# Kernel optimization log

Hardware: AMD Instinct MI355X
Metric: run time of the kernel (lower is better)

The kernel has to match this reference:

```python
import jax, jax.numpy as jnp
import numpy as np

ALPHA = 0.05   # propalpha
GDEP = 2       # gcn_depth
DIL = 2        # new_dilation
KSET = (2, 3, 6, 7)

def _dconv(x, w, b, d):
    # Conv2d(c_in, c_out, (1, k), dilation=(1, d), padding='same'), NCHW layout
    k = w.shape[-1]
    tot = d * (k - 1)
    lo = tot // 2
    y = jax.lax.conv_general_dilated(x, w, (1, 1), ((0, 0), (lo, tot - lo)),
                                     rhs_dilation=(1, d),
                                     dimension_numbers=('NCHW', 'OIHW', 'NCHW'))
    return y + b[None, :, None, None]

def _inception(x, ws, bs):
    # 'same' padding keeps seq_len for every branch, so the tail-slice is a no-op
    return jnp.concatenate([_dconv(x, w, b, DIL) for w, b in zip(ws, bs)], axis=1)

def _gcn(Hf, Aoff, W, b, n):
    # PyG GCNConv with unit edge weights (no edge_weight passed) and remaining self-loops:
    # out = D^-1/2 (A_off + I_R)^T D^-1/2 (Hf @ W^T) + b, where only rows < n carry edges.
    XW = Hf @ W.T
    deg = jnp.ones((Hf.shape[0],), Hf.dtype).at[:n].add(jnp.sum(Aoff, axis=0))
    dis = jax.lax.rsqrt(deg)
    out = XW / deg[:, None]                                           # self-loop term
    out = out.at[:n].add(dis[:n, None] * (Aoff.T @ (dis[:n, None] * XW[:n])))
    return out + b[None, :]

def _mixprop(X, A, gws, gbs, mw, mb):
    B, C, n, L = X.shape
    # dense_to_sparse ignores weights here (none passed to GCNConv) -> binary adjacency;
    # add_remaining_self_loops replaces any diagonal entries, so zero the diagonal.
    Aoff = (A != 0).astype(X.dtype) * (1.0 - jnp.eye(n, dtype=X.dtype))
    H = X
    hops = [X]
    for i in range(GDEP):
        Hf = H.reshape(B * L, C * n)   # torch row-major reshape, replicated exactly
        H1 = _gcn(Hf, Aoff, gws[i], gbs[i], n)
        H = ALPHA * X + H1.reshape(B, C, n, L)
        hops.append(H)
    Hc = jnp.concatenate(hops, axis=1)  # (B, (GDEP+1)*C, n, L)
    return jnp.einsum('bixl,oi->boxl', Hc, mw) + mb[None, :, None, None]

def _layernorm(x, w, b, idx, eps=1e-5):
    # F.layer_norm over all of x.shape[1:] with node-indexed affine params
    mu = jnp.mean(x, axis=(1, 2, 3), keepdims=True)
    var = jnp.var(x, axis=(1, 2, 3), keepdims=True)
    xh = (x - mu) * jax.lax.rsqrt(var + eps)
    return xh * w[:, idx, :][None] + b[:, idx, :][None]

def _forward(x, x_skip, A, idx, fws, fbs, gws, gbs, skip_w, skip_b,
             mp1_gw, mp1_gb, mp1_mw, mp1_mb, mp2_gw, mp2_gb, mp2_mw, mp2_mb,
             ln_w, ln_b):
    x_res = x
    xf = jnp.tanh(_inception(x, fws, fbs))
    xg = jax.nn.sigmoid(_inception(x, gws, gbs))
    x = xf * xg  # gated dilated temporal conv (dropout is an eval-mode no-op)
    x_skip = jnp.einsum('bixl,oi->boxl', x, skip_w) + skip_b[None, :, None, None] + x_skip
    x = (_mixprop(x, A, mp1_gw, mp1_gb, mp1_mw, mp1_mb)
         + _mixprop(x.swapaxes(0, 0), A.T, mp2_gw, mp2_gb, mp2_mw, mp2_mb))
    x = x + x_res[..., -x.shape[3]:]
    x = _layernorm(x, ln_w, ln_b, idx)
    return x, x_skip

def setup_inputs():
    key = jax.random.key(0)
    ks = jax.random.split(key, 32)
    B, C, N, L, SKIP = 16, 32, 128, 128, 64
    F = C * N
    co = C // len(KSET)
    d = {}
    d['x'] = jax.random.normal(ks[0], (B, C, N, L), jnp.float32)
    d['x_skip'] = jax.random.normal(ks[1], (B, SKIP, N, L), jnp.float32)
    d['A'] = jax.random.uniform(ks[2], (N, N), jnp.float32)
    d['idx'] = jnp.arange(N, dtype=jnp.int32)
    i = 3
    for pre in ('f', 'g'):
        for k in KSET:
            d[pre + 'w' + str(k)] = jax.random.normal(ks[i], (co, C, 1, k), jnp.float32) * float(1.0 / np.sqrt(C * k))
            d[pre + 'b' + str(k)] = jax.random.uniform(ks[i + 1], (co,), jnp.float32)
            i += 2
    d['skip_w'] = jax.random.normal(ks[i], (SKIP, C), jnp.float32) * float(1.0 / np.sqrt(C)); i += 1
    d['skip_b'] = jax.random.uniform(ks[i], (SKIP,), jnp.float32); i += 1
    for mp in ('mp1', 'mp2'):
        d[mp + '_gw'] = jax.random.normal(ks[i], (GDEP, F, F), jnp.float32) * float(1.0 / np.sqrt(F)); i += 1
        d[mp + '_gb'] = jnp.zeros((GDEP, F), jnp.float32)
        d[mp + '_mw'] = jax.random.normal(ks[i], (C, (GDEP + 1) * C), jnp.float32) * float(1.0 / np.sqrt((GDEP + 1) * C)); i += 1
        d[mp + '_mb'] = jax.random.uniform(ks[i], (C,), jnp.float32); i += 1
    d['ln_w'] = jnp.ones((C, N, L), jnp.float32)
    d['ln_b'] = jnp.zeros((C, N, L), jnp.float32)
    return d

def reference(x, x_skip, A, idx, fw2, fb2, fw3, fb3, fw6, fb6, fw7, fb7,
              gw2, gb2, gw3, gb3, gw6, gb6, gw7, gb7, skip_w, skip_b,
              mp1_gw, mp1_gb, mp1_mw, mp1_mb, mp2_gw, mp2_gb, mp2_mw, mp2_mb,
              ln_w, ln_b):
    return _forward(x, x_skip, A, idx,
                    [fw2, fw3, fw6, fw7], [fb2, fb3, fb6, fb7],
                    [gw2, gw3, gw6, gw7], [gb2, gb3, gb6, gb7],
                    skip_w, skip_b, mp1_gw, mp1_gb, mp1_mw, mp1_mb,
                    mp2_gw, mp2_gb, mp2_mw, mp2_mb, ln_w, ln_b)
```

## Files before the change

### kernel.cpp

```cpp
#include <hip/hip_runtime.h>
#include <stdint.h>

typedef unsigned short u16;
typedef unsigned int   u32;
typedef __attribute__((ext_vector_type(4))) float f32x4;
typedef __attribute__((ext_vector_type(8))) short bf16x8;

__device__ __forceinline__ u16 f2bf(float f) {
    u32 i = __float_as_uint(f);
    u32 r = (i + 0x7fffu + ((i >> 16) & 1u)) >> 16;
    return (u16)r;
}
__device__ __forceinline__ float bf2f(u16 u) {
    return __uint_as_float(((u32)u) << 16);
}
__device__ __forceinline__ u32 cvt2bf(float a, float b) {
    u32 r;
    asm("v_cvt_pk_bf16_f32 %0, %1, %2" : "=v"(r) : "v"(a), "v"(b));
    return r;
}

#define GLOAD16(g, l) __builtin_amdgcn_global_load_lds( \
    (const __attribute__((address_space(1))) void*)(g), \
    (__attribute__((address_space(3))) void*)(l), 16, 0, 0)

__global__ void k_prep(const float* __restrict__ A, float* dis1, float* inv1,
                       float* dis2, float* inv2)
{
    int r = threadIdx.x;
    if (r >= 128) return;
    int cc = 0, cr = 0;
    for (int j = 0; j < 128; ++j) {
        if (j == r) continue;
        if (A[(j << 7) + r] != 0.f) cc++;
        if (A[(r << 7) + j] != 0.f) cr++;
    }
    float d1 = 1.f + (float)cc, d2 = 1.f + (float)cr;
    dis1[r] = rsqrtf(d1); inv1[r] = 1.f / d1;
    dis2[r] = rsqrtf(d2); inv2[r] = 1.f / d2;
}

__global__ __launch_bounds__(256)
void k_wcvt2(const float* __restrict__ W0, const float* __restrict__ W1,
             u16* __restrict__ Wb0, u16* __restrict__ Wb1)
{
    int half = blockIdx.x >> 13;
    const float* W = half ? W1 : W0;
    u16* Wb = half ? Wb1 : Wb0;
    size_t e = ((size_t)(blockIdx.x & 8191) * 256 + threadIdx.x) * 8;
    f32x4 a = *(const f32x4*)(W + e);
    f32x4 b = *(const f32x4*)(W + e + 4);
    uint4 r;
    r.x = cvt2bf(a[0], a[1]); r.y = cvt2bf(a[2], a[3]);
    r.z = cvt2bf(b[0], b[1]); r.w = cvt2bf(b[2], b[3]);
    *(uint4*)(Wb + e) = r;
}

__global__ __launch_bounds__(512, 1)
void k_gemm2g(const u16* __restrict__ A0, const u16* __restrict__ A1,
              const u16* __restrict__ B0, const u16* __restrict__ B1,
              const u16* __restrict__ Gres,
              const float* __restrict__ gb0, const float* __restrict__ gb1,
              u16* __restrict__ Ha, u16* __restrict__ Hb,
              float* __restrict__ XW0a, float* __restrict__ XW0b)
{
    __shared__ alignas(16) u16 LDS[65536];
    const int NT = 128;
    const int tid  = threadIdx.x;
    const int lane = tid & 63;
    const int wid  = tid >> 6;
    const int wr = wid >> 2, wc = wid & 3;

    const int bid = blockIdx.x;
    const int swz = (bid & 7) * 32 + (bid >> 3);
    const int z   = swz >> 7;
    const int rem = swz & 127;
    const int bm = (rem >> 4) * 256;
    const int bn = (rem & 15) * 256;

    const u16* Ap = (z ? A1 : A0) + (size_t)bm * 4096;
    const u16* Bp = (z ? B1 : B0) + (size_t)bn * 4096;

    int aoff[8];
    #pragma unroll
    for (int i = 0; i < 8; ++i) {
        int ra = wr * 128 + i * 16 + (lane & 15);
        int sp = (lane >> 4) ^ ((ra >> 1) & 3);
        aoff[i] = ra * 32 + sp * 8;
    }
    int boff[4];
    #pragma unroll
    for (int j = 0; j < 4; ++j) {
        int rb = wc * 64 + j * 16 + (lane & 15);
        int sp = (lane >> 4) ^ ((rb >> 1) & 3);
        boff[j] = rb * 32 + sp * 8;
    }

    f32x4 acc[8][4] = {};

    auto stage = [&](int t) {
        const int k0  = t << 5;
        const int buf = (t & 3) << 14;
        #pragma unroll
        for (int h = 0; h < 2; ++h) {
            const int ch = tid + h * 512;
            const int r  = ch >> 2;
            const int sl = (ch & 3) ^ ((r >> 1) & 3);
            GLOAD16(Ap + (size_t)r * 4096 + k0 + sl * 8, LDS + buf + ch * 8);
            GLOAD16(Bp + (size_t)r * 4096 + k0 + sl * 8, LDS + buf + 8192 + ch * 8);
        }
    };
    auto compute = [&](int t) {
        const u16* base = LDS + ((t & 3) << 14);
        bf16x8 af[8], bv[4];
        #pragma unroll
        for (int i = 0; i < 8; ++i) af[i] = *(const bf16x8*)(base + aoff[i]);
        #pragma unroll
        for (int j = 0; j < 4; ++j) bv[j] = *(const bf16x8*)(base + 8192 + boff[j]);
        #pragma unroll
        for (int i = 0; i < 8; ++i)
            #pragma unroll
            for (int j = 0; j < 4; ++j)
                acc[i][j] = __builtin_amdgcn_mfma_f32_16x16x32_bf16(af[i], bv[j], acc[i][j], 0, 0, 0);
    };

    stage(0); stage(1); stage(2);
    asm volatile("s_waitcnt vmcnt(8)" ::: "memory");
    __syncthreads();

    int t = 0;
    for (; t < NT - 3; ++t) {
        stage(t + 3);
        compute(t);
        asm volatile("s_waitcnt vmcnt(8)" ::: "memory");
        __syncthreads();
    }
    compute(t);
    asm volatile("s_waitcnt vmcnt(4)" ::: "memory");
    __syncthreads(); ++t;
    compute(t);
    asm volatile("s_waitcnt vmcnt(0)" ::: "memory");
    __syncthreads(); ++t;
    compute(t);

    const int orow = (lane >> 4) * 4, ocol = lane & 15;
    const float* gbv = z ? gb1 : gb0;
    u16* H = z ? Hb : Ha;

    #pragma unroll
    for (int j = 0; j < 4; ++j) {
        const int o = bn + wc * 64 + j * 16 + ocol;
        const float gbo = gbv[o];
        #pragma unroll
        for (int i = 0; i < 8; ++i) {
            const int rbase = bm + wr * 128 + i * 16 + orow;
            #pragma unroll
            for (int v = 0; v < 4; ++v) {
                const size_t e = (size_t)(rbase + v) * 4096 + o;
                float g = bf2f(Gres[e]);
                H[e] = f2bf(__fmaf_rn(0.05f, g, acc[i][j][v] + gbo));
            }
        }
    }
    if (bm == 0 && wr == 0) {
        float* XW0 = z ? XW0b : XW0a;
        #pragma unroll
        for (int i = 0; i < 8; ++i) {
            #pragma unroll
            for (int j = 0; j < 4; ++j) {
                float* cp = XW0 + (size_t)(i * 16 + orow) * 4096 + (bn + wc * 64 + j * 16 + ocol);
                #pragma unroll
                for (int v = 0; v < 4; ++v)
                    cp[(size_t)v * 4096] = acc[i][j][v];
            }
        }
    }
}

__global__ __launch_bounds__(256)
void k_gcnfix(const float* __restrict__ XW0a, const float* __restrict__ XW0b,
              const u16* __restrict__ G, const float* __restrict__ Af,
              const float* __restrict__ dis1, const float* __restrict__ inv1,
              const float* __restrict__ dis2, const float* __restrict__ inv2,
              const float* __restrict__ gb0, const float* __restrict__ gb1,
              u16* __restrict__ Ha, u16* __restrict__ Hb)
{
    const int prob = blockIdx.x >> 9;
    const int rem  = blockIdx.x & 511;
    const int t4 = rem * 256 + threadIdx.x;
    const int r = t4 >> 10, og = (t4 & 1023) << 2;
    const float* XW0 = prob ? XW0b : XW0a;
    const float* dis = prob ? dis2 : dis1;
    const float* inv = prob ? inv2 : inv1;
    const float* gb  = prob ? gb1  : gb0;
    u16* H = prob ? Hb : Ha;

    const size_t e = ((size_t)r << 12) + og;
    f32x4 xw = *(const f32x4*)(XW0 + e);
    f32x4 s = {0.f, 0.f, 0.f, 0.f};
    for (int j = 0; j < 128; ++j) {
        float av = prob ? Af[(r << 7) + j] : Af[(j << 7) + r];
        float wv = ((av != 0.f) && (j != r)) ? dis[j] : 0.f;
        f32x4 xv = *(const f32x4*)(XW0 + ((size_t)j << 12) + og);
        #pragma unroll
        for (int q = 0; q < 4; ++q) s[q] = __fmaf_rn(wv, xv[q], s[q]);
    }
    const float iv = inv[r], dr = dis[r];
    f32x4 gb4 = *(const f32x4*)(gb + og);
    uint2 gv = *(const uint2*)(G + e);
    float g0 = __uint_as_float(gv.x << 16), g1 = __uint_as_float(gv.x & 0xffff0000u);
    float g2 = __uint_as_float(gv.y << 16), g3 = __uint_as_float(gv.y & 0xffff0000u);
    float y0 = __fmaf_rn(0.05f, g0, __fmaf_rn(dr, s[0], xw[0] * iv) + gb4[0]);
    float y1 = __fmaf_rn(0.05f, g1, __fmaf_rn(dr, s[1], xw[1] * iv) + gb4[1]);
    float y2 = __fmaf_rn(0.05f, g2, __fmaf_rn(dr, s[2], xw[2] * iv) + gb4[2]);
    float y3 = __fmaf_rn(0.05f, g3, __fmaf_rn(dr, s[3], xw[3] * iv) + gb4[3]);
    uint2 rr;
    rr.x = cvt2bf(y0, y1);
    rr.y = cvt2bf(y2, y3);
    *(uint2*)(H + e) = rr;
}

__device__ __forceinline__ constexpr int wbase_of(int k) {
    return k == 2 ? 0 : k == 3 ? 520 : k == 6 ? 1296 : 2840;
}
__device__ __forceinline__ constexpr int ob_of(int k) {
    return k == 2 ? 0 : k == 3 ? 8 : k == 6 ? 16 : 24;
}

template<int K_>
__device__ __forceinline__ void conv_phase(const float* __restrict__ xsb,
                                           const float* __restrict__ wfp,
                                           const float* __restrict__ wgp,
                                           float fb, float gb,
                                           u16* __restrict__ Gp)
{
    float accf[8], accg[8];
    #pragma unroll
    for (int i = 0; i < 8; ++i) { accf[i] = fb; accg[i] = gb; }
    for (int c = 0; c < 32; ++c) {
        float xw[24];
        const float* xr = xsb + c * 144;
        #pragma unroll
        for (int q = 0; q < 6; ++q) {
            f32x4 v = *(const f32x4*)(xr + q * 4);
            xw[q * 4 + 0] = v[0]; xw[q * 4 + 1] = v[1];
            xw[q * 4 + 2] = v[2]; xw[q * 4 + 3] = v[3];
        }
        float wfj[K_], wgj[K_];
        const float* wfc = wfp + c * K_;
        const float* wgc = wgp + c * K_;
        #pragma unroll
        for (int j = 0; j < K_; ++j) { wfj[j] = wfc[j]; wgj[j] = wgc[j]; }
        #pragma unroll
        for (int li = 0; li < 8; ++li) {
            #pragma unroll
            for (int j = 0; j < K_; ++j) {
                float xv = xw[li + 8 - (K_ - 1) + 2 * j];
                accf[li] = __fmaf_rn(xv, wfj[j], accf[li]);
                accg[li] = __fmaf_rn(xv, wgj[j], accg[li]);
            }
        }
    }
    u16 o8[8];
    #pragma unroll
    for (int i = 0; i < 8; ++i) {
        float e2 = __expf(2.f * accf[i]);
        float th = 1.f - __fdividef(2.f, e2 + 1.f);
        float sg = __fdividef(1.f, 1.f + __expf(-accg[i]));
        o8[i] = f2bf(th * sg);
    }
    uint4 u;
    u.x = o8[0] | ((u32)o8[1] << 16); u.y = o8[2] | ((u32)o8[3] << 16);
    u.z = o8[4] | ((u32)o8[5] << 16); u.w = o8[6] | ((u32)o8[7] << 16);
    *(uint4*)Gp = u;
}

template<int KA, int KB>
__device__ __forceinline__ void wave_pair(const float* __restrict__ xs,
                                          const float* __restrict__ wfl,
                                          const float* __restrict__ wgl,
                                          const float* __restrict__ fbl,
                                          const float* __restrict__ gbl,
                                          int oo, int lL, int b, int n,
                                          u16* __restrict__ G)
{
    {
        constexpr int BS = wbase_of(KA), ST = 32 * KA + 1, OB = ob_of(KA);
        const int o = OB + oo, l0 = lL * 8;
        conv_phase<KA>(xs + l0, wfl + BS + oo * ST, wgl + BS + oo * ST,
                       fbl[o], gbl[o],
                       G + (((size_t)(b * 32 + o) * 128 + n) * 128 + l0));
    }
    {
        constexpr int BS = wbase_of(KB), ST = 32 * KB + 1, OB = ob_of(KB);
        const int o = OB + oo, l0 = 64 + lL * 8;
        conv_phase<KB>(xs + l0, wfl + BS + oo * ST, wgl + BS + oo * ST,
                       fbl[o], gbl[o],
                       G + (((size_t)(b * 32 + o) * 128 + n) * 128 + l0));
    }
}

__global__ __launch_bounds__(256)
void k_incep(const float* __restrict__ x,
             const float* __restrict__ fw2p, const float* __restrict__ fw3p,
             const float* __restrict__ fw6p, const float* __restrict__ fw7p,
             const float* __restrict__ fb2p, const float* __restrict__ fb3p,
             const float* __restrict__ fb6p, const float* __restrict__ fb7p,
             const float* __restrict__ gw2p, const float* __restrict__ gw3p,
             const float* __restrict__ gw6p, const float* __restrict__ gw7p,
             const float* __restrict__ gb2p, const float* __restrict__ gb3p,
             const float* __restrict__ gb6p, const float* __restrict__ gb7p,
             u16* __restrict__ G)
{
    __shared__ alignas(16) float xs[32 * 144];
    __shared__ float wfl[4640], wgl[4640];
    __shared__ float fbl[32], gbl[32];
    const int tid = threadIdx.x;
    const int b = blockIdx.x >> 7, n = blockIdx.x & 127;

    for (int i = tid; i < 32 * 144; i += 256) xs[i] = 0.f;
    for (int g = tid; g < 4608; g += 256) {
        int rel, k, woff;
        const float *pf, *pg;
        if (g < 512)       { rel = g;        k = 2; woff = 0;    pf = fw2p; pg = gw2p; }
        else if (g < 1280) { rel = g - 512;  k = 3; woff = 520;  pf = fw3p; pg = gw3p; }
        else if (g < 2816) { rel = g - 1280; k = 6; woff = 1296; pf = fw6p; pg = gw6p; }
        else               { rel = g - 2816; k = 7; woff = 2840; pf = fw7p; pg = gw7p; }
        int ck = 32 * k;
        int oo = rel / ck, rem = rel % ck;
        int dst = woff + oo * (ck + 1) + rem;
        wfl[dst] = pf[rel];
        wgl[dst] = pg[rel];
    }
    if (tid < 32) {
        int br = tid >> 3, oo = tid & 7;
        const float* pf = br == 0 ? fb2p : br == 1 ? fb3p : br == 2 ? fb6p : fb7p;
        const float* pg = br == 0 ? gb2p : br == 1 ? gb3p : br == 2 ? gb6p : gb7p;
        fbl[tid] = pf[oo]; gbl[tid] = pg[oo];
    }
    __syncthreads();
    const float* xb = x + (size_t)b * 524288 + n * 128;
    for (int p = 0; p < 4; ++p) {
        int chunk = p * 256 + tid;
        int c = chunk >> 5, l4 = (chunk & 31) * 4;
        *(f32x4*)&xs[c * 144 + 8 + l4] = *(const f32x4*)(xb + (size_t)c * 16384 + l4);
    }
    __syncthreads();

    const int w = tid >> 6, lane = tid & 63;
    const int oo = lane >> 3, lL = lane & 7;
    switch (w) {
        case 0:  wave_pair<2, 7>(xs, wfl, wgl, fbl, gbl, oo, lL, b, n, G); break;
        case 1:  wave_pair<7, 2>(xs, wfl, wgl, fbl, gbl, oo, lL, b, n, G); break;
        case 2:  wave_pair<3, 6>(xs, wfl, wgl, fbl, gbl, oo, lL, b, n, G); break;
        default: wave_pair<6, 3>(xs, wfl, wgl, fbl, gbl, oo, lL, b, n, G); break;
    }
}

__global__ __launch_bounds__(256)
void k_skip(const u16* __restrict__ G, const float* __restrict__ xskip,
            const float* __restrict__ sw, const float* __restrict__ sb,
            float* __restrict__ outp)
{
    __shared__ alignas(16) u16 Gs[4096];
    __shared__ float swl[64 * 33];
    __shared__ float sbl[64];
    const int tid = threadIdx.x;
    const int b = blockIdx.x >> 7, n = blockIdx.x & 127;
    const u16* gb_ = G + (size_t)b * 524288 + n * 128;
    for (int p = 0; p < 2; ++p) {
        int chunk = p * 256 + tid, c = chunk >> 4, l8 = (chunk & 15) * 8;
        *(uint4*)&Gs[c * 128 + l8] = *(const uint4*)(gb_ + (size_t)c * 16384 + l8);
    }
    for (int i = tid; i < 2048; i += 256) swl[(i >> 5) * 33 + (i & 31)] = sw[i];
    if (tid < 64) sbl[tid] = sb[tid];
    __syncthreads();
    const int sg = (tid & 15) * 4, l0 = (tid >> 4) * 8;
    float acc[4][8];
    #pragma unroll
    for (int si = 0; si < 4; ++si) {
        float bv = sbl[sg + si];
        #pragma unroll
        for (int li = 0; li < 8; ++li) acc[si][li] = bv;
    }
    for (int c = 0; c < 32; ++c) {
        uint4 gv = *(const uint4*)&Gs[c * 128 + l0];
        float g[8];
        g[0] = __uint_as_float(gv.x << 16); g[1] = __uint_as_float(gv.x & 0xffff0000u);
        g[2] = __uint_as_float(gv.y << 16); g[3] = __uint_as_float(gv.y & 0xffff0000u);
        g[4] = __uint_as_float(gv.z << 16); g[5] = __uint_as_float(gv.z & 0xffff0000u);
        g[6] = __uint_as_float(gv.w << 16); g[7] = __uint_as_float(gv.w & 0xffff0000u);
        #pragma unroll
        for (int si = 0; si < 4; ++si) {
            float wv = swl[(sg + si) * 33 + c];
            #pragma unroll
            for (int li = 0; li < 8; ++li) acc[si][li] = __fmaf_rn(g[li], wv, acc[si][li]);
        }
    }
    #pragma unroll
    for (int si = 0; si < 4; ++si) {
        size_t e = ((size_t)(b * 64 + sg + si) * 128 + n) * 128 + l0;
        f32x4 x0 = *(const f32x4*)(xskip + e);
        f32x4 x1 = *(const f32x4*)(xskip + e + 4);
        f32x4 r0, r1;
        r0[0] = acc[si][0] + x0[0]; r0[1] = acc[si][1] + x0[1];
        r0[2] = acc[si][2] + x0[2]; r0[3] = acc[si][3] + x0[3];
        r1[0] = acc[si][4] + x1[0]; r1[1] = acc[si][5] + x1[1];
        r1[2] = acc[si][6] + x1[2]; r1[3] = acc[si][7] + x1[3];
        *(f32x4*)(outp + e)     = r0;
        *(f32x4*)(outp + e + 4) = r1;
    }
}

__global__ __launch_bounds__(256)
void k_mix2ln(const u16* __restrict__ G,
              const u16* __restrict__ H1, const u16* __restrict__ H2,
              const u16* __restrict__ H1b, const u16* __restrict__ H2b,
              const float* __restrict__ mw1, const float* __restrict__ mb1,
              const float* __restrict__ mw2, const float* __restrict__ mb2,
              const float* __restrict__ x,
              float* __restrict__ Y, float* __restrict__ partial)
{
    __shared__ alignas(16) u16 Gs[4096], H1s[4096], H2s[4096], H1bs[4096], H2bs[4096];
    __shared__ float wSg[32 * 33], wS11[32 * 33], wS12[32 * 33], wS21[32 * 33], wS22[32 * 33];
    __shared__ float mbl[32];
    const int tid = threadIdx.x;
    const int b = blockIdx.x >> 7, xn = blockIdx.x & 127;
    size_t base = (size_t)b * 524288 + xn * 128;
    for (int p = 0; p < 2; ++p) {
        int chunk = p * 256 + tid, c = chunk >> 4, l8 = (chunk & 15) * 8;
        size_t src = base + (size_t)c * 16384 + l8;
        *(uint4*)&Gs[c * 128 + l8]   = *(const uint4*)(G + src);
        *(uint4*)&H1s[c * 128 + l8]  = *(const uint4*)(H1 + src);
        *(uint4*)&H2s[c * 128 + l8]  = *(const uint4*)(H2 + src);
        *(uint4*)&H1bs[c * 128 + l8] = *(const uint4*)(H1b + src);
        *(uint4*)&H2bs[c * 128 + l8] = *(const uint4*)(H2b + src);
    }
    for (int i = tid; i < 1024; i += 256) {
        int o = i >> 5, c = i & 31;
        int d = o * 33 + c;
        wSg[d]  = mw1[o * 96 + c] + mw2[o * 96 + c];
        wS11[d] = mw1[o * 96 + 32 + c];
        wS12[d] = mw1[o * 96 + 64 + c];
        wS21[d] = mw2[o * 96 + 32 + c];
        wS22[d] = mw2[o * 96 + 64 + c];
    }
    if (tid < 32) mbl[tid] = mb1[tid] + mb2[tid];
    __syncthreads();
    const int og = (tid & 7) * 4, l0 = (tid >> 3) * 4;
    float acc[4][4];
    #pragma unroll
    for (int oi = 0; oi < 4; ++oi) {
        float bv = mbl[og + oi];
        acc[oi][0] = bv; acc[oi][1] = bv; acc[oi][2] = bv; acc[oi][3] = bv;
    }
    for (int c = 0; c < 32; ++c) {
        uint2 ga = *(const uint2*)&Gs[c * 128 + l0];
        uint2 h1 = *(const uint2*)&H1s[c * 128 + l0];
        uint2 h2 = *(const uint2*)&H2s[c * 128 + l0];
        uint2 j1 = *(const uint2*)&H1bs[c * 128 + l0];
        uint2 j2 = *(const uint2*)&H2bs[c * 128 + l0];
        float gv[4], v1[4], v2[4], u1[4], u2[4];
        gv[0] = __uint_as_float(ga.x << 16); gv[1] = __uint_as_float(ga.x & 0xffff0000u);
        gv[2] = __uint_as_float(ga.y << 16); gv[3] = __uint_as_float(ga.y & 0xffff0000u);
        v1[0] = __uint_as_float(h1.x << 16); v1[1] = __uint_as_float(h1.x & 0xffff0000u);
        v1[2] = __uint_as_float(h1.y << 16); v1[3] = __uint_as_float(h1.y & 0xffff0000u);
        v2[0] = __uint_as_float(h2.x << 16); v2[1] = __uint_as_float(h2.x & 0xffff0000u);
        v2[2] = __uint_as_float(h2.y << 16); v2[3] = __uint_as_float(h2.y & 0xffff0000u);
        u1[0] = __uint_as_float(j1.x << 16); u1[1] = __uint_as_float(j1.x & 0xffff0000u);
        u1[2] = __uint_as_float(j1.y << 16); u1[3] = __uint_as_float(j1.y & 0xffff0000u);
        u2[0] = __uint_as_float(j2.x << 16); u2[1] = __uint_as_float(j2.x & 0xffff0000u);
        u2[2] = __uint_as_float(j2.y << 16); u2[3] = __uint_as_float(j2.y & 0xffff0000u);
        #pragma unroll
        for (int oi = 0; oi < 4; ++oi) {
            int d = (og + oi) * 33 + c;
            float a0 = wSg[d], a1 = wS11[d], a2 = wS12[d], a3 = wS21[d], a4 = wS22[d];
            #pragma unroll
            for (int li = 0; li < 4; ++li)
                acc[oi][li] += gv[li] * a0 + v1[li] * a1 + v2[li] * a2
                             + u1[li] * a3 + u2[li] * a4;
        }
    }
    float s = 0.f, ss = 0.f;
    #pragma unroll
    for (int oi = 0; oi < 4; ++oi) {
        size_t e = ((size_t)(b * 32 + og + oi) * 128 + xn) * 128 + l0;
        f32x4 xv = *(const f32x4*)(x + e);
        f32x4 yv;
        #pragma unroll
        for (int li = 0; li < 4; ++li) {
            float y = acc[oi][li] + xv[li];
            yv[li] = y;
            s += y; ss += y * y;
        }
        *(f32x4*)(Y + e) = yv;
    }
    #pragma unroll
    for (int o = 32; o > 0; o >>= 1) {
        s  += __shfl_down(s,  o, 64);
        ss += __shfl_down(ss, o, 64);
    }
    __shared__ float sred[8];
    int w = tid >> 6;
    if ((tid & 63) == 0) { sred[w * 2] = s; sred[w * 2 + 1] = ss; }
    __syncthreads();
    if (tid == 0) {
        partial[blockIdx.x * 2]     = sred[0] + sred[2] + sred[4] + sred[6];
        partial[blockIdx.x * 2 + 1] = sred[1] + sred[3] + sred[5] + sred[7];
    }
}

__global__ __launch_bounds__(256)
void k_lnnorm(const float* __restrict__ Y,
              const float* __restrict__ partial, const int* __restrict__ idxp,
              const float* __restrict__ lnw, const float* __restrict__ lnb,
              float* __restrict__ outx)
{
    const int tid = threadIdx.x;
    const int b = blockIdx.x >> 7, chunk = blockIdx.x & 127;
    float s = 0.f, ss = 0.f;
    if (tid < 128) {
        s  = partial[(b * 128 + tid) * 2];
        ss = partial[(b * 128 + tid) * 2 + 1];
    }
    #pragma unroll
    for (int o = 32; o > 0; o >>= 1) {
        s  += __shfl_down(s,  o, 64);
        ss += __shfl_down(ss, o, 64);
    }
    __shared__ float sred[4];
    __shared__ float mv[2];
    if ((tid & 63) == 0 && tid < 128) { sred[(tid >> 6) * 2] = s; sred[(tid >> 6) * 2 + 1] = ss; }
    __syncthreads();
    if (tid == 0) {
        float S = sred[0] + sred[2], SS = sred[1] + sred[3];
        float mean = S * (1.f / 524288.f);
        float var = SS * (1.f / 524288.f) - mean * mean;
        mv[0] = mean; mv[1] = rsqrtf(var + 1e-5f);
    }
    __syncthreads();
    const float mean = mv[0], rstd = mv[1];
    #pragma unroll
    for (int q = 0; q < 4; ++q) {
        int ib = chunk * 4096 + q * 1024 + tid * 4;
        size_t e = (size_t)b * 524288 + ib;
        f32x4 yv = *(const f32x4*)(Y + e);
        int c = ib >> 14, xn = (ib >> 7) & 127, l = ib & 127;
        int ix = idxp[xn];
        size_t we = ((size_t)c * 128 + ix) * 128 + l;
        f32x4 wv = *(const f32x4*)(lnw + we);
        f32x4 bv = *(const f32x4*)(lnb + we);
        f32x4 r;
        #pragma unroll
        for (int j = 0; j < 4; ++j)
            r[j] = (yv[j] - mean) * rstd * wv[j] + bv[j];
        *(f32x4*)(outx + e) = r;
    }
}

extern "C" void kernel_launch(void* const* d_in, const int* in_sizes, int n_in,
                              void* d_out, int out_size, void* d_ws, size_t ws_size,
                              hipStream_t stream)
{
    (void)in_sizes; (void)n_in; (void)out_size; (void)ws_size;
    const float* x      = (const float*)d_in[0];
    const float* xskip  = (const float*)d_in[1];
    const float* A      = (const float*)d_in[2];
    const int*   idxp   = (const int*)d_in[3];
    const float* fw2p = (const float*)d_in[4];  const float* fb2p = (const float*)d_in[5];
    const float* fw3p = (const float*)d_in[6];  const float* fb3p = (const float*)d_in[7];
    const float* fw6p = (const float*)d_in[8];  const float* fb6p = (const float*)d_in[9];
    const float* fw7p = (const float*)d_in[10]; const float* fb7p = (const float*)d_in[11];
    const float* gw2p = (const float*)d_in[12]; const float* gb2p = (const float*)d_in[13];
    const float* gw3p = (const float*)d_in[14]; const float* gb3p = (const float*)d_in[15];
    const float* gw6p = (const float*)d_in[16]; const float* gb6p = (const float*)d_in[17];
    const float* gw7p = (const float*)d_in[18]; const float* gb7p = (const float*)d_in[19];
    const float* sw   = (const float*)d_in[20]; const float* sb   = (const float*)d_in[21];
    const float* mp1_gw = (const float*)d_in[22]; const float* mp1_gb = (const float*)d_in[23];
    const float* mp1_mw = (const float*)d_in[24]; const float* mp1_mb = (const float*)d_in[25];
    const float* mp2_gw = (const float*)d_in[26]; const float* mp2_gb = (const float*)d_in[27];
    const float* mp2_mw = (const float*)d_in[28]; const float* mp2_mb = (const float*)d_in[29];
    const float* lnw = (const float*)d_in[30]; const float* lnb = (const float*)d_in[31];

    char* wsb = (char*)d_ws;
    float* out_x  = (float*)d_out;
    float* out_sk = out_x + 8388608;

    const size_t MB16 = 16777216, MB33 = 33554432;
    u16*   G    = (u16*)(wsb);
    u16*   H1   = (u16*)(wsb + MB16);
    u16*   H1b  = (u16*)(wsb + 2 * MB16);
    u16*   H2   = (u16*)(wsb + 3 * MB16);
    u16*   H2b  = (u16*)(wsb + 4 * MB16);
    u16*   Wb0  = (u16*)(wsb + 5 * MB16);
    u16*   Wb1  = (u16*)(wsb + 5 * MB16 + MB33);
    float* Yb   = (float*)Wb0;
    float* XW0a = (float*)(wsb + 5 * MB16 + 2 * MB33);
    float* XW0b = (float*)(wsb + 5 * MB16 + 2 * MB33 + 2097152);
    float* part = (float*)(wsb + 5 * MB16 + 2 * MB33 + 4194304);
    float* dd   = (float*)(wsb + 5 * MB16 + 2 * MB33 + 4194304 + 16384);
    float *dis1 = dd, *inv1 = dd + 128, *dis2 = dd + 256, *inv2 = dd + 384;

    k_prep<<<1, 128, 0, stream>>>(A, dis1, inv1, dis2, inv2);
    k_incep<<<2048, 256, 0, stream>>>(x, fw2p, fw3p, fw6p, fw7p, fb2p, fb3p, fb6p, fb7p,
                                      gw2p, gw3p, gw6p, gw7p, gb2p, gb3p, gb6p, gb7p, G);
    k_skip<<<2048, 256, 0, stream>>>(G, xskip, sw, sb, out_sk);

    k_wcvt2<<<16384, 256, 0, stream>>>(mp1_gw, mp2_gw, Wb0, Wb1);
    k_gemm2g<<<256, 512, 0, stream>>>(G, G, Wb0, Wb1, G, mp1_gb, mp2_gb,
                                      H1, H1b, XW0a, XW0b);
    k_gcnfix<<<1024, 256, 0, stream>>>(XW0a, XW0b, G, A, dis1, inv1, dis2, inv2,
                                       mp1_gb, mp2_gb, H1, H1b);
    k_wcvt2<<<16384, 256, 0, stream>>>(mp1_gw + MB16, mp2_gw + MB16, Wb0, Wb1);
    k_gemm2g<<<256, 512, 0, stream>>>(H1, H1b, Wb0, Wb1, G, mp1_gb + 4096, mp2_gb + 4096,
                                      H2, H2b, XW0a, XW0b);
    k_gcnfix<<<1024, 256, 0, stream>>>(XW0a, XW0b, G, A, dis1, inv1, dis2, inv2,
                                       mp1_gb + 4096, mp2_gb + 4096, H2, H2b);
    k_mix2ln<<<2048, 256, 0, stream>>>(G, H1, H2, H1b, H2b, mp1_mw, mp1_mb,
                                       mp2_mw, mp2_mb, x, Yb, part);
    k_lnnorm<<<2048, 256, 0, stream>>>(Yb, part, idxp, lnw, lnb, out_x);
}
```

Baseline: 719.7 us.

## Restructure GEMM main loop into 64-wide K steps with interleaved quarter-tile loads

Replaces the 4-stage 32-wide K pipeline in the fused GCN GEMM with a double-buffered 64-wide K step. Each step is split into four MFMA phases, and each phase issues part of the next tiles' global-to-LDS loads between LDS fragment reads and compute. Raw s_barrier calls and s_setprio around the MFMA bursts aim to overlap memory traffic with matrix work and to keep waves in lockstep, ping-pong style. This adds more barriers per iteration and tight vmcnt accounting, which is fragile if the load counts do not line up.

```diff
diff --git a/kernel.cpp b/kernel.cpp
--- a/kernel.cpp
+++ b/kernel.cpp
@@ -23,6 +23,9 @@
 #define GLOAD16(g, l) __builtin_amdgcn_global_load_lds( \
     (const __attribute__((address_space(1))) void*)(g), \
     (__attribute__((address_space(3))) void*)(l), 16, 0, 0)
+
+#define RAW_BARRIER()  asm volatile("s_barrier" ::: "memory")
+#define VMCNT(n)       asm volatile("s_waitcnt vmcnt(" #n ")" ::: "memory")
 
 __global__ void k_prep(const float* __restrict__ A, float* dis1, float* inv1,
                        float* dis2, float* inv2)
@@ -65,7 +68,7 @@
               float* __restrict__ XW0a, float* __restrict__ XW0b)
 {
     __shared__ alignas(16) u16 LDS[65536];
-    const int NT = 128;
+    const int NT = 64;
     const int tid  = threadIdx.x;
     const int lane = tid & 63;
     const int wid  = tid >> 6;
@@ -81,67 +84,124 @@
     const u16* Ap = (z ? A1 : A0) + (size_t)bm * 4096;
     const u16* Bp = (z ? B1 : B0) + (size_t)bn * 4096;
 
-    int aoff[8];
+    int aoff[8], boff[4];
     #pragma unroll
     for (int i = 0; i < 8; ++i) {
-        int ra = wr * 128 + i * 16 + (lane & 15);
-        int sp = (lane >> 4) ^ ((ra >> 1) & 3);
-        aoff[i] = ra * 32 + sp * 8;
-    }
-    int boff[4];
+        int row = wr * 128 + i * 16 + (lane & 15);
+        int sp  = (lane >> 4) ^ ((row >> 1) & 3);
+        aoff[i] = row * 32 + sp * 8;
+    }
     #pragma unroll
     for (int j = 0; j < 4; ++j) {
-        int rb = wc * 64 + j * 16 + (lane & 15);
-        int sp = (lane >> 4) ^ ((rb >> 1) & 3);
-        boff[j] = rb * 32 + sp * 8;
-    }
+        int row = wc * 64 + j * 16 + (lane & 15);
+        int sp  = (lane >> 4) ^ ((row >> 1) & 3);
+        boff[j] = row * 32 + sp * 8;
+    }
+
+    auto stageA = [&](int t, int kh) {
+        if (t >= NT) return;
+        const int kb = t * 64 + kh * 32;
+        u16* dst = LDS + ((t & 1) << 15) + (kh << 13);
+        #pragma unroll
+        for (int h = 0; h < 2; ++h) {
+            const int c = tid + h * 512;
+            const int r = c >> 2;
+            const int sl = (c & 3) ^ ((r >> 1) & 3);
+            GLOAD16(Ap + (size_t)r * 4096 + kb + sl * 8, dst + c * 8);
+        }
+    };
+    auto stageB = [&](int t, int kh) {
+        if (t >= NT) return;
+        const int kb = t * 64 + kh * 32;
+        u16* dst = LDS + ((t & 1) << 15) + 16384 + (kh << 13);
+        #pragma unroll
+        for (int h = 0; h < 2; ++h) {
+            const int c = tid + h * 512;
+            const int r = c >> 2;
+            const int sl = (c & 3) ^ ((r >> 1) & 3);
+            GLOAD16(Bp + (size_t)r * 4096 + kb + sl * 8, dst + c * 8);
+        }
+    };
 
     f32x4 acc[8][4] = {};
 
-    auto stage = [&](int t) {
-        const int k0  = t << 5;
-        const int buf = (t & 3) << 14;
-        #pragma unroll
-        for (int h = 0; h < 2; ++h) {
-            const int ch = tid + h * 512;
-            const int r  = ch >> 2;
-            const int sl = (ch & 3) ^ ((r >> 1) & 3);
-            GLOAD16(Ap + (size_t)r * 4096 + k0 + sl * 8, LDS + buf + ch * 8);
-            GLOAD16(Bp + (size_t)r * 4096 + k0 + sl * 8, LDS + buf + 8192 + ch * 8);
-        }
-    };
-    auto compute = [&](int t) {
-        const u16* base = LDS + ((t & 3) << 14);
-        bf16x8 af[8], bv[4];
-        #pragma unroll
-        for (int i = 0; i < 8; ++i) af[i] = *(const bf16x8*)(base + aoff[i]);
-        #pragma unroll
-        for (int j = 0; j < 4; ++j) bv[j] = *(const bf16x8*)(base + 8192 + boff[j]);
-        #pragma unroll
-        for (int i = 0; i < 8; ++i)
-            #pragma unroll
-            for (int j = 0; j < 4; ++j)
-                acc[i][j] = __builtin_amdgcn_mfma_f32_16x16x32_bf16(af[i], bv[j], acc[i][j], 0, 0, 0);
-    };
-
-    stage(0); stage(1); stage(2);
-    asm volatile("s_waitcnt vmcnt(8)" ::: "memory");
-    __syncthreads();
-
-    int t = 0;
-    for (; t < NT - 3; ++t) {
-        stage(t + 3);
-        compute(t);
-        asm volatile("s_waitcnt vmcnt(8)" ::: "memory");
-        __syncthreads();
-    }
-    compute(t);
-    asm volatile("s_waitcnt vmcnt(4)" ::: "memory");
-    __syncthreads(); ++t;
-    compute(t);
-    asm volatile("s_waitcnt vmcnt(0)" ::: "memory");
-    __syncthreads(); ++t;
-    compute(t);
+    stageA(0, 0); stageB(0, 0); stageA(0, 1); stageB(0, 1);
+    stageA(1, 0); stageB(1, 0);
+    VMCNT(0);
+    RAW_BARRIER();
+
+    for (int t = 0; t < NT; ++t) {
+        const int bb = (t & 1) << 15;
+        bf16x8 bfr[4];
+        {
+            bf16x8 afr[4];
+            #pragma unroll
+            for (int i = 0; i < 4; ++i) afr[i] = *(const bf16x8*)(LDS + bb + aoff[i]);
+            #pragma unroll
+            for (int j = 0; j < 4; ++j) bfr[j] = *(const bf16x8*)(LDS + bb + 16384 + boff[j]);
+            stageA(t + 1, 1);
+            VMCNT(8);
+            RAW_BARRIER();
+            __builtin_amdgcn_s_setprio(1);
+            #pragma unroll
+            for (int i = 0; i < 4; ++i)
+                #pragma unroll
+                for (int j = 0; j < 4; ++j)
+                    acc[i][j] = __builtin_amdgcn_mfma_f32_16x16x32_bf16(afr[i], bfr[j], acc[i][j], 0, 0, 0);
+            __builtin_amdgcn_s_setprio(0);
+            RAW_BARRIER();
+        }
+        {
+            bf16x8 afr[4];
+            #pragma unroll
+            for (int i = 0; i < 4; ++i) afr[i] = *(const bf16x8*)(LDS + bb + aoff[i + 4]);
+            stageB(t + 1, 1);
+            VMCNT(8);
+            RAW_BARRIER();
+            __builtin_amdgcn_s_setprio(1);
+            #pragma unroll
+            for (int i = 0; i < 4; ++i)
+                #pragma unroll
+                for (int j = 0; j < 4; ++j)
+                    acc[i + 4][j] = __builtin_amdgcn_mfma_f32_16x16x32_bf16(afr[i], bfr[j], acc[i + 4][j], 0, 0, 0);
+            __builtin_amdgcn_s_setprio(0);
+            RAW_BARRIER();
+        }
+        {
+            bf16x8 afr[4];
+            #pragma unroll
+            for (int i = 0; i < 4; ++i) afr[i] = *(const bf16x8*)(LDS + bb + 8192 + aoff[i]);
+            #pragma unroll
+            for (int j = 0; j < 4; ++j) bfr[j] = *(const bf16x8*)(LDS + bb + 24576 + boff[j]);
+            stageA(t + 2, 0);
+            VMCNT(8);
+            RAW_BARRIER();
+            __builtin_amdgcn_s_setprio(1);
+            #pragma unroll
+            for (int i = 0; i < 4; ++i)
+                #pragma unroll
+                for (int j = 0; j < 4; ++j)
+                    acc[i][j] = __builtin_amdgcn_mfma_f32_16x16x32_bf16(afr[i], bfr[j], acc[i][j], 0, 0, 0);
+            __builtin_amdgcn_s_setprio(0);
+            RAW_BARRIER();
+        }
+        {
+            bf16x8 afr[4];
+            #pragma unroll
+            for (int i = 0; i < 4; ++i) afr[i] = *(const bf16x8*)(LDS + bb + 8192 + aoff[i + 4]);
+            stageB(t + 2, 0);
+            VMCNT(8);
+            RAW_BARRIER();
+            __builtin_amdgcn_s_setprio(1);
+            #pragma unroll
+            for (int i = 0; i < 4; ++i)
+                #pragma unroll
+                for (int j = 0; j < 4; ++j)
+                    acc[i + 4][j] = __builtin_amdgcn_mfma_f32_16x16x32_bf16(afr[i], bfr[j], acc[i + 4][j], 0, 0, 0);
+            __builtin_amdgcn_s_setprio(0);
+            RAW_BARRIER();
+        }
+    }
 
     const int orow = (lane >> 4) * 4, ocol = lane & 15;
     const float* gbv = z ? gb1 : gb0;
```

After: 671.0 us. -6.8%, faster.
